# Kernel tuning notes

Hardware: AMD Instinct MI355X
Metric: run time of the kernel (lower is better)

## Reference

```python
import jax, jax.numpy as jnp
import numpy as np

N_NODES = 50000
N_EDGES = 800000
NUM_HEADS = 4
HEAD_DIM = 32
IN_DIM = 128
NEG_SLOPE = 0.2


def setup_inputs() -> dict:
    key = jax.random.key(0)
    k1, k2, k3, k4, k5, k6 = jax.random.split(key, 6)
    x = jax.random.normal(k1, (N_NODES, IN_DIM), dtype=jnp.float32)
    W = jax.random.normal(k2, (NUM_HEADS * HEAD_DIM, IN_DIM), dtype=jnp.float32) * 0.05
    attn_l = jax.random.normal(k3, (NUM_HEADS, HEAD_DIM), dtype=jnp.float32) * 0.05
    attn_r = jax.random.normal(k4, (NUM_HEADS, HEAD_DIM), dtype=jnp.float32) * 0.05
    src = jax.random.randint(k5, (N_EDGES,), 0, N_NODES, dtype=jnp.int32)
    dst = jnp.sort(jax.random.randint(k6, (N_EDGES,), 0, N_NODES, dtype=jnp.int32))
    return {"x": x, "W": W, "attn_l": attn_l, "attn_r": attn_r, "src": src, "dst": dst}


def reference(x, W, attn_l, attn_r, src, dst):
    N = x.shape[0]
    H, D = attn_l.shape
    # linear projection: [N, H*D] -> [N, H, D]
    feat = (x @ W.T).reshape(N, H, D)
    # per-node attention terms  [N, H]
    el = jnp.einsum('nhd,hd->nh', feat, attn_l)
    er = jnp.einsum('nhd,hd->nh', feat, attn_r)
    # per-edge logits (u_add_v) + leaky relu  [E, H]
    e = el[src] + er[dst]
    e = jnp.where(e > 0, e, NEG_SLOPE * e)
    # edge softmax segmented by destination node
    e_max = jax.ops.segment_max(e, dst, num_segments=N)          # [N, H]
    e_exp = jnp.exp(e - e_max[dst])                              # [E, H]
    denom = jax.ops.segment_sum(e_exp, dst, num_segments=N)     # [N, H]
    alpha = e_exp / denom[dst]                                   # [E, H]
    # attention-weighted neighbor aggregation  [N, H, D]
    out = jax.ops.segment_sum(alpha[:, :, None] * feat[src], dst, num_segments=N)
    return out.reshape(N, H * D)
```

## Files before the change

### kernel.cpp

```cpp
#include <hip/hip_runtime.h>
#include <math.h>

#define NN 50000
#define NE 800000
#define NH 4
#define HD 32
#define FD 128
#define NTILE 3125
#define GEMM_BLOCKS 512
#define ROWS_BLOCKS ((NE + 511) / 512)
#define CAP 1024

typedef __attribute__((ext_vector_type(8))) short short8;
typedef __attribute__((ext_vector_type(4))) float floatx4;

__device__ __forceinline__ unsigned short f2bf(float f) {
    union { float f; unsigned u; } v; v.f = f;
    unsigned u = v.u;
    return (unsigned short)((u + 0x7FFFu + ((u >> 16) & 1u)) >> 16);
}
__device__ __forceinline__ float bfu(unsigned short u) {
    union { unsigned u; float f; } v; v.u = (unsigned)u << 16; return v.f;
}
__device__ __forceinline__ float bf_lo(unsigned u) {
    union { unsigned u; float f; } v; v.u = u << 16; return v.f;
}
__device__ __forceinline__ float bf_hi(unsigned u) {
    union { unsigned u; float f; } v; v.u = u & 0xFFFF0000u; return v.f;
}

__global__ __launch_bounds__(512) void k_gemm_rows(const float* __restrict__ x,
                                                   const float* __restrict__ W,
                                                   const float* __restrict__ al,
                                                   const float* __restrict__ ar,
                                                   const int* __restrict__ dst,
                                                   unsigned short* __restrict__ feat_bf,
                                                   float* __restrict__ el,
                                                   float* __restrict__ er,
                                                   int* __restrict__ rows) {
    const int tid = threadIdx.x;

    if (blockIdx.x >= GEMM_BLOCKS) {
        int e = (blockIdx.x - GEMM_BLOCKS) * 512 + tid;
        if (e < NE) {
            int dj = dst[e];
            if (e == 0) {
                for (int n = 0; n <= dj; ++n) rows[n] = 0;
            } else {
                int prev = dst[e - 1];
                for (int n = prev + 1; n <= dj; ++n) rows[n] = e;
            }
            if (e == NE - 1) {
                for (int n = dj + 1; n <= NN; ++n) rows[n] = NE;
            }
        }
        return;
    }

    __shared__ unsigned short Wl[FD * 136];
    __shared__ unsigned short WaL[16 * 136];
    __shared__ float aS[2 * FD];

    for (int p = tid; p < FD * 64; p += 512) {
        int c = p >> 6, k2 = (p & 63) * 2;
        float2 wv = *(const float2*)&W[c * FD + k2];
        *(unsigned*)&Wl[c * 136 + k2] =
            (unsigned)f2bf(wv.x) | ((unsigned)f2bf(wv.y) << 16);
    }
    if (tid < FD) aS[tid] = al[tid];
    else if (tid < 2 * FD) aS[tid] = ar[tid - FD];
    __syncthreads();

    for (int p = tid; p < 16 * FD; p += 512) {
        int c = p >> 7, k = p & 127;
        float v = 0.f;
        if (c < 8) {
            int h = c & 3;
            const float* av = &aS[(c >> 2) * FD + h * HD];
            const unsigned short* wl = &Wl[h * HD * 136 + k];
            #pragma unroll 8
            for (int d = 0; d < HD; ++d) v += bfu(wl[d * 136]) * av[d];
        }
        WaL[c * 136 + k] = f2bf(v);
    }
    __syncthreads();

    const int wv_id = tid >> 6, lane = tid & 63;
    const int col = lane & 15, quad = lane >> 4;

    for (int tile = blockIdx.x * 8 + wv_id; tile < NTILE; tile += GEMM_BLOCKS * 8) {
        const int n0 = tile * 16;

        short8 afrag[4];
        const float* xrow = x + (size_t)(n0 + col) * FD;
        #pragma unroll
        for (int s = 0; s < 4; ++s) {
            float4 u0 = *(const float4*)&xrow[s * 32 + quad * 8];
            float4 u1 = *(const float4*)&xrow[s * 32 + quad * 8 + 4];
            short8 a;
            a[0] = (short)f2bf(u0.x); a[1] = (short)f2bf(u0.y);
            a[2] = (short)f2bf(u0.z); a[3] = (short)f2bf(u0.w);
            a[4] = (short)f2bf(u1.x); a[5] = (short)f2bf(u1.y);
            a[6] = (short)f2bf(u1.z); a[7] = (short)f2bf(u1.w);
            afrag[s] = a;
        }

        floatx4 acc[8], acce;
        #pragma unroll
        for (int ct = 0; ct < 8; ++ct) acc[ct] = (floatx4){0.f, 0.f, 0.f, 0.f};
        acce = (floatx4){0.f, 0.f, 0.f, 0.f};

        #pragma unroll
        for (int ct = 0; ct < 8; ++ct) {
            #pragma unroll
            for (int s = 0; s < 4; ++s) {
                short8 b = *(const short8*)&Wl[(ct * 16 + col) * 136 + s * 32 + quad * 8];
                acc[ct] = __builtin_amdgcn_mfma_f32_16x16x32_bf16(afrag[s], b, acc[ct], 0, 0, 0);
            }
        }
        #pragma unroll
        for (int s = 0; s < 4; ++s) {
            short8 b = *(const short8*)&WaL[col * 136 + s * 32 + quad * 8];
            acce = __builtin_amdgcn_mfma_f32_16x16x32_bf16(afrag[s], b, acce, 0, 0, 0);
        }

        #pragma unroll
        for (int ct = 0; ct < 8; ++ct) {
            #pragma unroll
            for (int r = 0; r < 4; ++r) {
                feat_bf[(size_t)(n0 + quad * 4 + r) * FD + ct * 16 + col] = f2bf(acc[ct][r]);
            }
        }
        #pragma unroll
        for (int r = 0; r < 4; ++r) {
            int n = n0 + quad * 4 + r;
            if (col < 4)      el[n * NH + col]     = acce[r];
            else if (col < 8) er[n * NH + col - 4] = acce[r];
        }
    }
}

__global__ __launch_bounds__(256) void k_aggregate(const unsigned short* __restrict__ feat_bf,
                                                   const float* __restrict__ el,
                                                   const float* __restrict__ er,
                                                   const int* __restrict__ src,
                                                   const int* __restrict__ dst,
                                                   const int* __restrict__ rows,
                                                   float* __restrict__ out) {
    __shared__ float wS[CAP * NH];
    __shared__ int   sS[CAP];
    const int tid = threadIdx.x;
    const int wave = tid >> 6;
    const int lane = tid & 63;
    const int n0 = blockIdx.x * 4;
    const int n  = n0 + wave;

    const int s0 = __builtin_amdgcn_readfirstlane(rows[n0]);
    const int t3 = __builtin_amdgcn_readfirstlane(rows[n0 + 4]);
    const int s  = __builtin_amdgcn_readfirstlane(rows[n]);
    const int t  = __builtin_amdgcn_readfirstlane(rows[n + 1]);

    const int q  = lane >> 4;
    const int lp = lane & 15;
    const int h  = lp >> 2;
    const int dimoff = 8 * lp;

    float acc[8] = {0.f, 0.f, 0.f, 0.f, 0.f, 0.f, 0.f, 0.f};
    float den = 0.f;

    for (int c0 = s0; c0 < t3; c0 += CAP) {
        const int c1 = min(c0 + CAP, t3);

        for (int e = c0 + tid; e < c1; e += 256) {
            int sj = src[e], dj = dst[e];
            sS[e - c0] = sj;
            float4 l4 = *(const float4*)&el[sj * NH];
            float4 r4 = *(const float4*)&er[dj * NH];
            float4 w; float lg;
            lg = l4.x + r4.x; w.x = __expf(fmaxf(lg, 0.2f * lg));
            lg = l4.y + r4.y; w.y = __expf(fmaxf(lg, 0.2f * lg));
            lg = l4.z + r4.z; w.z = __expf(fmaxf(lg, 0.2f * lg));
            lg = l4.w + r4.w; w.w = __expf(fmaxf(lg, 0.2f * lg));
            *(float4*)&wS[(e - c0) * NH] = w;
        }
        __syncthreads();

        const int sb = max(s, c0), tb = min(t, c1);
        for (int e = sb; e < tb; e += 16) {
            const int base = e + 4 * q;
            float wv4[4];
            int   sj4[4];
            uint4 uvv[4];
            #pragma unroll
            for (int u = 0; u < 4; ++u) {
                int ei = base + u;
                bool v = ei < tb;
                int ii = v ? (ei - c0) : 0;
                sj4[u] = sS[ii];
                wv4[u] = v ? wS[ii * NH + h] : 0.f;
                if (v) uvv[u] = *(const uint4*)&feat_bf[(size_t)sj4[u] * FD + dimoff];
            }
            #pragma unroll
            for (int u = 0; u < 4; ++u) {
                int ei = base + u;
                if (ei < tb) {
                    float w = wv4[u];
                    uint4 uv = uvv[u];
                    acc[0] += w * bf_lo(uv.x); acc[1] += w * bf_hi(uv.x);
                    acc[2] += w * bf_lo(uv.y); acc[3] += w * bf_hi(uv.y);
                    acc[4] += w * bf_lo(uv.z); acc[5] += w * bf_hi(uv.z);
                    acc[6] += w * bf_lo(uv.w); acc[7] += w * bf_hi(uv.w);
                    den += w;
                }
            }
        }
        __syncthreads();
    }

    #pragma unroll
    for (int m = 16; m < 64; m <<= 1) {
        #pragma unroll
        for (int j = 0; j < 8; ++j) acc[j] += __shfl_xor(acc[j], m);
        den += __shfl_xor(den, m);
    }

    if (q == 0) {
        const float rden = (den > 0.f) ? 1.f / den : 0.f;
        float* op = out + (size_t)n * FD + dimoff;
        *(float4*)op       = make_float4(acc[0] * rden, acc[1] * rden, acc[2] * rden, acc[3] * rden);
        *(float4*)(op + 4) = make_float4(acc[4] * rden, acc[5] * rden, acc[6] * rden, acc[7] * rden);
    }
}

extern "C" void kernel_launch(void* const* d_in, const int* in_sizes, int n_in,
                              void* d_out, int out_size, void* d_ws, size_t ws_size,
                              hipStream_t stream) {
    const float* x  = (const float*)d_in[0];
    const float* W  = (const float*)d_in[1];
    const float* al = (const float*)d_in[2];
    const float* ar = (const float*)d_in[3];
    const int* src  = (const int*)d_in[4];
    const int* dst  = (const int*)d_in[5];
    float* out = (float*)d_out;

    unsigned short* feat_bf = (unsigned short*)d_ws;
    float* el = (float*)(feat_bf + (size_t)NN * FD);
    float* er = el + (size_t)NN * NH;
    int*   rows = (int*)(er + (size_t)NN * NH);

    k_gemm_rows<<<GEMM_BLOCKS + ROWS_BLOCKS, 512, 0, stream>>>(x, W, al, ar, dst,
                                                               feat_bf, el, er, rows);
    k_aggregate<<<NN / 4, 256, 0, stream>>>(feat_bf, el, er, src, dst, rows, out);
}
```

Before: 130.8 us.

## Process sixteen destination nodes per block, four per wave sequentially

The aggregate kernel now assigns 16 destination nodes per block, and each wave walks 4 nodes in sequence, writing each node's output when its edge range ends inside the current chunk. Row offsets are staged once in shared memory, and the shared edge-weight chunk is filled cooperatively for all 16 nodes. This cuts the block count by four and amortizes block setup and synchronization over more edges. In exchange, each wave does serial work with more per-node reductions, and there is more load imbalance across waves and less parallelism per node.

```diff
diff --git a/kernel.cpp b/kernel.cpp
--- a/kernel.cpp
+++ b/kernel.cpp
@@ -9,7 +9,9 @@
 #define NTILE 3125
 #define GEMM_BLOCKS 512
 #define ROWS_BLOCKS ((NE + 511) / 512)
-#define CAP 1024
+#define NPB 16
+#define NPW 4
+#define CAP 1008
 
 typedef __attribute__((ext_vector_type(8))) short short8;
 typedef __attribute__((ext_vector_type(4))) float floatx4;
@@ -149,27 +151,33 @@
                                                    float* __restrict__ out) {
     __shared__ float wS[CAP * NH];
     __shared__ int   sS[CAP];
+    __shared__ int   rS[NPB + 1];
     const int tid = threadIdx.x;
     const int wave = tid >> 6;
     const int lane = tid & 63;
-    const int n0 = blockIdx.x * 4;
-    const int n  = n0 + wave;
-
-    const int s0 = __builtin_amdgcn_readfirstlane(rows[n0]);
-    const int t3 = __builtin_amdgcn_readfirstlane(rows[n0 + 4]);
-    const int s  = __builtin_amdgcn_readfirstlane(rows[n]);
-    const int t  = __builtin_amdgcn_readfirstlane(rows[n + 1]);
+    const int n0 = blockIdx.x * NPB;
+
+    if (tid <= NPB) rS[tid] = rows[n0 + tid];
+    __syncthreads();
+
+    const int s0 = rS[0];
+    const int tE = rS[NPB];
 
     const int q  = lane >> 4;
     const int lp = lane & 15;
     const int h  = lp >> 2;
     const int dimoff = 8 * lp;
 
+    int gsv[NPW + 1];
+    #pragma unroll
+    for (int i = 0; i <= NPW; ++i) gsv[i] = rS[wave * NPW + i];
+
     float acc[8] = {0.f, 0.f, 0.f, 0.f, 0.f, 0.f, 0.f, 0.f};
     float den = 0.f;
-
-    for (int c0 = s0; c0 < t3; c0 += CAP) {
-        const int c1 = min(c0 + CAP, t3);
+    int ni = 0;
+
+    for (int c0 = s0; c0 < tE; c0 += CAP) {
+        const int c1 = min(c0 + CAP, tE);
 
         for (int e = c0 + tid; e < c1; e += 256) {
             int sj = src[e], dj = dst[e];
@@ -185,50 +193,57 @@
         }
         __syncthreads();
 
-        const int sb = max(s, c0), tb = min(t, c1);
-        for (int e = sb; e < tb; e += 16) {
-            const int base = e + 4 * q;
-            float wv4[4];
-            int   sj4[4];
-            uint4 uvv[4];
-            #pragma unroll
-            for (int u = 0; u < 4; ++u) {
-                int ei = base + u;
-                bool v = ei < tb;
-                int ii = v ? (ei - c0) : 0;
-                sj4[u] = sS[ii];
-                wv4[u] = v ? wS[ii * NH + h] : 0.f;
-                if (v) uvv[u] = *(const uint4*)&feat_bf[(size_t)sj4[u] * FD + dimoff];
-            }
-            #pragma unroll
-            for (int u = 0; u < 4; ++u) {
-                int ei = base + u;
-                if (ei < tb) {
-                    float w = wv4[u];
-                    uint4 uv = uvv[u];
-                    acc[0] += w * bf_lo(uv.x); acc[1] += w * bf_hi(uv.x);
-                    acc[2] += w * bf_lo(uv.y); acc[3] += w * bf_hi(uv.y);
-                    acc[4] += w * bf_lo(uv.z); acc[5] += w * bf_hi(uv.z);
-                    acc[6] += w * bf_lo(uv.w); acc[7] += w * bf_hi(uv.w);
-                    den += w;
+        while (ni < NPW) {
+            const int gs = gsv[ni], ge = gsv[ni + 1];
+            const int sb = max(gs, c0), tb = min(ge, c1);
+            for (int e = sb; e < tb; e += 16) {
+                const int base = e + 4 * q;
+                float wv4[4];
+                int   sj4[4];
+                uint4 uvv[4];
+                #pragma unroll
+                for (int u = 0; u < 4; ++u) {
+                    int ei = base + u;
+                    bool v = ei < tb;
+                    int ii = v ? (ei - c0) : 0;
+                    sj4[u] = sS[ii];
+                    wv4[u] = v ? wS[ii * NH + h] : 0.f;
+                    if (v) uvv[u] = *(const uint4*)&feat_bf[(size_t)sj4[u] * FD + dimoff];
                 }
-            }
+                #pragma unroll
+                for (int u = 0; u < 4; ++u) {
+                    int ei = base + u;
+                    if (ei < tb) {
+                        float w = wv4[u];
+                        uint4 uv = uvv[u];
+                        acc[0] += w * bf_lo(uv.x); acc[1] += w * bf_hi(uv.x);
+                        acc[2] += w * bf_lo(uv.y); acc[3] += w * bf_hi(uv.y);
+                        acc[4] += w * bf_lo(uv.z); acc[5] += w * bf_hi(uv.z);
+                        acc[6] += w * bf_lo(uv.w); acc[7] += w * bf_hi(uv.w);
+                        den += w;
+                    }
+                }
+            }
+            if (ge > c1) break;
+
+            #pragma unroll
+            for (int m = 16; m < 64; m <<= 1) {
+                #pragma unroll
+                for (int j = 0; j < 8; ++j) acc[j] += __shfl_xor(acc[j], m);
+                den += __shfl_xor(den, m);
+            }
+            if (q == 0) {
+                const float rden = (den > 0.f) ? 1.f / den : 0.f;
+                float* op = out + (size_t)(n0 + wave * NPW + ni) * FD + dimoff;
+                *(float4*)op       = make_float4(acc[0] * rden, acc[1] * rden, acc[2] * rden, acc[3] * rden);
+                *(float4*)(op + 4) = make_float4(acc[4] * rden, acc[5] * rden, acc[6] * rden, acc[7] * rden);
+            }
+            #pragma unroll
+            for (int j = 0; j < 8; ++j) acc[j] = 0.f;
+            den = 0.f;
+            ++ni;
         }
         __syncthreads();
-    }
-
-    #pragma unroll
-    for (int m = 16; m < 64; m <<= 1) {
-        #pragma unroll
-        for (int j = 0; j < 8; ++j) acc[j] += __shfl_xor(acc[j], m);
-        den += __shfl_xor(den, m);
-    }
-
-    if (q == 0) {
-        const float rden = (den > 0.f) ? 1.f / den : 0.f;
-        float* op = out + (size_t)n * FD + dimoff;
-        *(float4*)op       = make_float4(acc[0] * rden, acc[1] * rden, acc[2] * rden, acc[3] * rden);
-        *(float4*)(op + 4) = make_float4(acc[4] * rden, acc[5] * rden, acc[6] * rden, acc[7] * rden);
     }
 }
 
@@ -250,5 +265,5 @@
 
     k_gemm_rows<<<GEMM_BLOCKS + ROWS_BLOCKS, 512, 0, stream>>>(x, W, al, ar, dst,
                                                                feat_bf, el, er, rows);
-    k_aggregate<<<NN / 4, 256, 0, stream>>>(feat_bf, el, er, src, dst, rows, out);
-}
+    k_aggregate<<<NN / NPB, 256, 0, stream>>>(feat_bf, el, er, src, dst, rows, out);
+}
```

Result: slower. 135.8 us (+3.8%).

## Make aggregate kernel persistent with double-buffered prefetch of next node group

Applied to the files above, without the earlier changes.

The aggregation kernel now launches a fixed grid of 2048 blocks that loop over node groups instead of one block per 4 nodes. While gathering features for the current group, each block prefetches the src/dst indices and el/er terms for its next group, then computes the exp weights into a second shared-memory buffer. Groups with more than 256 edges fall back to computing weights directly from global memory. This aims to hide index and attention-term load latency and cut block launch overhead, at the cost of fewer resident blocks to hide gather latency and extra register pressure.

```diff
diff --git a/kernel.cpp b/kernel.cpp
--- a/kernel.cpp
+++ b/kernel.cpp
@@ -9,7 +9,9 @@
 #define NTILE 3125
 #define GEMM_BLOCKS 512
 #define ROWS_BLOCKS ((NE + 511) / 512)
-#define CAP 1024
+#define NG 12500
+#define AGG_BLOCKS 2048
+#define GCAP 256
 
 typedef __attribute__((ext_vector_type(8))) short short8;
 typedef __attribute__((ext_vector_type(4))) float floatx4;
@@ -147,88 +149,134 @@
                                                    const int* __restrict__ dst,
                                                    const int* __restrict__ rows,
                                                    float* __restrict__ out) {
-    __shared__ float wS[CAP * NH];
-    __shared__ int   sS[CAP];
+    __shared__ float wS[2][GCAP * NH];
+    __shared__ int   sS[2][GCAP];
     const int tid = threadIdx.x;
-    const int wave = tid >> 6;
-    const int lane = tid & 63;
-    const int n0 = blockIdx.x * 4;
-    const int n  = n0 + wave;
-
-    const int s0 = __builtin_amdgcn_readfirstlane(rows[n0]);
-    const int t3 = __builtin_amdgcn_readfirstlane(rows[n0 + 4]);
-    const int s  = __builtin_amdgcn_readfirstlane(rows[n]);
-    const int t  = __builtin_amdgcn_readfirstlane(rows[n + 1]);
-
-    const int q  = lane >> 4;
-    const int lp = lane & 15;
-    const int h  = lp >> 2;
+    const int wave = tid >> 6, lane = tid & 63;
+    const int q = lane >> 4, lp = lane & 15, h = lp >> 2;
     const int dimoff = 8 * lp;
 
-    float acc[8] = {0.f, 0.f, 0.f, 0.f, 0.f, 0.f, 0.f, 0.f};
-    float den = 0.f;
-
-    for (int c0 = s0; c0 < t3; c0 += CAP) {
-        const int c1 = min(c0 + CAP, t3);
-
-        for (int e = c0 + tid; e < c1; e += 256) {
-            int sj = src[e], dj = dst[e];
-            sS[e - c0] = sj;
-            float4 l4 = *(const float4*)&el[sj * NH];
-            float4 r4 = *(const float4*)&er[dj * NH];
+    int g = blockIdx.x;
+
+    int s0  = __builtin_amdgcn_readfirstlane(rows[g * 4]);
+    int t3  = __builtin_amdgcn_readfirstlane(rows[g * 4 + 4]);
+    int cnt = t3 - s0;
+    if (cnt <= GCAP && s0 + tid < t3) {
+        int sj = src[s0 + tid], dj = dst[s0 + tid];
+        sS[0][tid] = sj;
+        float4 l4 = *(const float4*)&el[sj * NH];
+        float4 r4 = *(const float4*)&er[dj * NH];
+        float4 w; float lg;
+        lg = l4.x + r4.x; w.x = __expf(fmaxf(lg, 0.2f * lg));
+        lg = l4.y + r4.y; w.y = __expf(fmaxf(lg, 0.2f * lg));
+        lg = l4.z + r4.z; w.z = __expf(fmaxf(lg, 0.2f * lg));
+        lg = l4.w + r4.w; w.w = __expf(fmaxf(lg, 0.2f * lg));
+        *(float4*)&wS[0][tid * NH] = w;
+    }
+    __syncthreads();
+
+    int buf = 0;
+    for (; g < NG; g += AGG_BLOCKS) {
+        const int nxt = g + AGG_BLOCKS;
+
+        int ns0 = 0, nt3 = 0, ncnt = 0, nsj = 0;
+        float4 nl4 = make_float4(0.f, 0.f, 0.f, 0.f);
+        float4 nr4 = make_float4(0.f, 0.f, 0.f, 0.f);
+        bool mv = false;
+        if (nxt < NG) {
+            ns0  = __builtin_amdgcn_readfirstlane(rows[nxt * 4]);
+            nt3  = __builtin_amdgcn_readfirstlane(rows[nxt * 4 + 4]);
+            ncnt = nt3 - ns0;
+            if (ncnt <= GCAP && ns0 + tid < nt3) {
+                mv = true;
+                int dj = dst[ns0 + tid];
+                nsj = src[ns0 + tid];
+                nl4 = *(const float4*)&el[nsj * NH];
+                nr4 = *(const float4*)&er[dj * NH];
+            }
+        }
+
+        const int n = g * 4 + wave;
+        const int s = __builtin_amdgcn_readfirstlane(rows[n]);
+        const int t = __builtin_amdgcn_readfirstlane(rows[n + 1]);
+        float acc[8] = {0.f, 0.f, 0.f, 0.f, 0.f, 0.f, 0.f, 0.f};
+        float den = 0.f;
+
+        if (cnt <= GCAP) {
+            for (int e = s; e < t; e += 16) {
+                const int base = e + 4 * q;
+                float wv4[4];
+                int   sj4[4];
+                uint4 uvv[4];
+                #pragma unroll
+                for (int u = 0; u < 4; ++u) {
+                    int ei = base + u;
+                    bool v = ei < t;
+                    int ii = v ? (ei - s0) : 0;
+                    sj4[u] = sS[buf][ii];
+                    wv4[u] = v ? wS[buf][ii * NH + h] : 0.f;
+                    if (v) uvv[u] = *(const uint4*)&feat_bf[(size_t)sj4[u] * FD + dimoff];
+                }
+                #pragma unroll
+                for (int u = 0; u < 4; ++u) {
+                    if (base + u < t) {
+                        float w = wv4[u];
+                        uint4 uv = uvv[u];
+                        acc[0] += w * bf_lo(uv.x); acc[1] += w * bf_hi(uv.x);
+                        acc[2] += w * bf_lo(uv.y); acc[3] += w * bf_hi(uv.y);
+                        acc[4] += w * bf_lo(uv.z); acc[5] += w * bf_hi(uv.z);
+                        acc[6] += w * bf_lo(uv.w); acc[7] += w * bf_hi(uv.w);
+                        den += w;
+                    }
+                }
+            }
+        } else {
+            for (int e = s; e < t; e += 16) {
+                const int base = e + 4 * q;
+                #pragma unroll
+                for (int u = 0; u < 4; ++u) {
+                    int ei = base + u;
+                    if (ei < t) {
+                        int sj = src[ei];
+                        float lg = el[sj * NH + h] + er[n * NH + h];
+                        float w = __expf(fmaxf(lg, 0.2f * lg));
+                        uint4 uv = *(const uint4*)&feat_bf[(size_t)sj * FD + dimoff];
+                        acc[0] += w * bf_lo(uv.x); acc[1] += w * bf_hi(uv.x);
+                        acc[2] += w * bf_lo(uv.y); acc[3] += w * bf_hi(uv.y);
+                        acc[4] += w * bf_lo(uv.z); acc[5] += w * bf_hi(uv.z);
+                        acc[6] += w * bf_lo(uv.w); acc[7] += w * bf_hi(uv.w);
+                        den += w;
+                    }
+                }
+            }
+        }
+
+        #pragma unroll
+        for (int m = 16; m < 64; m <<= 1) {
+            #pragma unroll
+            for (int j = 0; j < 8; ++j) acc[j] += __shfl_xor(acc[j], m);
+            den += __shfl_xor(den, m);
+        }
+        if (q == 0) {
+            const float rden = (den > 0.f) ? 1.f / den : 0.f;
+            float* op = out + (size_t)n * FD + dimoff;
+            *(float4*)op       = make_float4(acc[0] * rden, acc[1] * rden, acc[2] * rden, acc[3] * rden);
+            *(float4*)(op + 4) = make_float4(acc[4] * rden, acc[5] * rden, acc[6] * rden, acc[7] * rden);
+        }
+
+        if (mv) {
+            sS[buf ^ 1][tid] = nsj;
             float4 w; float lg;
-            lg = l4.x + r4.x; w.x = __expf(fmaxf(lg, 0.2f * lg));
-            lg = l4.y + r4.y; w.y = __expf(fmaxf(lg, 0.2f * lg));
-            lg = l4.z + r4.z; w.z = __expf(fmaxf(lg, 0.2f * lg));
-            lg = l4.w + r4.w; w.w = __expf(fmaxf(lg, 0.2f * lg));
-            *(float4*)&wS[(e - c0) * NH] = w;
-        }
+            lg = nl4.x + nr4.x; w.x = __expf(fmaxf(lg, 0.2f * lg));
+            lg = nl4.y + nr4.y; w.y = __expf(fmaxf(lg, 0.2f * lg));
+            lg = nl4.z + nr4.z; w.z = __expf(fmaxf(lg, 0.2f * lg));
+            lg = nl4.w + nr4.w; w.w = __expf(fmaxf(lg, 0.2f * lg));
+            *(float4*)&wS[buf ^ 1][tid * NH] = w;
+        }
+
         __syncthreads();
-
-        const int sb = max(s, c0), tb = min(t, c1);
-        for (int e = sb; e < tb; e += 16) {
-            const int base = e + 4 * q;
-            float wv4[4];
-            int   sj4[4];
-            uint4 uvv[4];
-            #pragma unroll
-            for (int u = 0; u < 4; ++u) {
-                int ei = base + u;
-                bool v = ei < tb;
-                int ii = v ? (ei - c0) : 0;
-                sj4[u] = sS[ii];
-                wv4[u] = v ? wS[ii * NH + h] : 0.f;
-                if (v) uvv[u] = *(const uint4*)&feat_bf[(size_t)sj4[u] * FD + dimoff];
-            }
-            #pragma unroll
-            for (int u = 0; u < 4; ++u) {
-                int ei = base + u;
-                if (ei < tb) {
-                    float w = wv4[u];
-                    uint4 uv = uvv[u];
-                    acc[0] += w * bf_lo(uv.x); acc[1] += w * bf_hi(uv.x);
-                    acc[2] += w * bf_lo(uv.y); acc[3] += w * bf_hi(uv.y);
-                    acc[4] += w * bf_lo(uv.z); acc[5] += w * bf_hi(uv.z);
-                    acc[6] += w * bf_lo(uv.w); acc[7] += w * bf_hi(uv.w);
-                    den += w;
-                }
-            }
-        }
-        __syncthreads();
-    }
-
-    #pragma unroll
-    for (int m = 16; m < 64; m <<= 1) {
-        #pragma unroll
-        for (int j = 0; j < 8; ++j) acc[j] += __shfl_xor(acc[j], m);
-        den += __shfl_xor(den, m);
-    }
-
-    if (q == 0) {
-        const float rden = (den > 0.f) ? 1.f / den : 0.f;
-        float* op = out + (size_t)n * FD + dimoff;
-        *(float4*)op       = make_float4(acc[0] * rden, acc[1] * rden, acc[2] * rden, acc[3] * rden);
-        *(float4*)(op + 4) = make_float4(acc[4] * rden, acc[5] * rden, acc[6] * rden, acc[7] * rden);
+        buf ^= 1;
+        s0 = ns0; t3 = nt3; cnt = ncnt;
     }
 }
 
@@ -250,5 +298,5 @@
 
     k_gemm_rows<<<GEMM_BLOCKS + ROWS_BLOCKS, 512, 0, stream>>>(x, W, al, ar, dst,
                                                                feat_bf, el, er, rows);
-    k_aggregate<<<NN / 4, 256, 0, stream>>>(feat_bf, el, er, src, dst, rows, out);
-}
+    k_aggregate<<<AGG_BLOCKS, 256, 0, stream>>>(feat_bf, el, er, src, dst, rows, out);
+}
```

New measurement: 146.9 us. 12.3% more time.
